# Performance work log

Hardware: AMD Instinct MI355X
Metric: run time of the kernel (lower is better)

The kernel has to match this reference:

```python
import jax, jax.numpy as jnp
import numpy as np

B, S, D, H, NUM_REL = 8, 1024, 1024, 16, 512
HD = D // H  # head size = 64


def setup_inputs() -> dict:
    key = jax.random.key(0)
    ks = jax.random.split(key, 12)
    sc = 0.02  # weight init scale for numerical stability
    inp = {
        "query": jax.random.normal(ks[0], (B, S, D), jnp.float32),
        "key": jax.random.normal(ks[1], (B, S, D), jnp.float32),
        "value": jax.random.normal(ks[2], (B, S, D), jnp.float32),
        "Wq": jax.random.normal(ks[3], (D, D), jnp.float32) * sc,
        "bq": jnp.zeros((D,), jnp.float32),
        "Wk": jax.random.normal(ks[4], (D, D), jnp.float32) * sc,
        "bk": jnp.zeros((D,), jnp.float32),
        "Wv": jax.random.normal(ks[5], (D, D), jnp.float32) * sc,
        "bv": jnp.zeros((D,), jnp.float32),
        "Wo": jax.random.normal(ks[6], (D, D), jnp.float32) * sc,
        "bo": jnp.zeros((D,), jnp.float32),
        "pos_table": jax.random.normal(ks[7], (NUM_REL, HD), jnp.float32) * sc,
        # True = masked position (causal: cannot attend to future)
        "mask": jnp.broadcast_to(jnp.triu(jnp.ones((S, S), bool), k=1), (B, S, S)),
    }
    return inp


def reference(query, key, value, Wq, bq, Wk, bk, Wv, bv, Wo, bo, pos_table, mask):
    Bq, Sq, Dm = query.shape
    hd = Dm // H

    def proj(x, W, b):
        # nn.Linear: x @ W.T + b, then split heads -> [B, H, S, hd]
        return (x @ W.T + b).reshape(Bq, Sq, H, hd).transpose(0, 2, 1, 3)

    q = proj(query, Wq, bq)
    k = proj(key, Wk, bk)
    v = proj(value, Wv, bv)

    scores = jnp.einsum("bhid,bhjd->bhij", q, k)

    # relative-position bias: idxs[i,j] = clip(i - j, 0, NUM_REL-1)
    t = jnp.arange(Sq)
    idxs = jnp.clip(t[:, None] - t[None, :], 0, pos_table.shape[0] - 1)
    pos = pos_table[idxs]  # [S, S, hd]
    scores = scores + jnp.einsum("bhid,ijd->bhij", q, pos)

    scores = scores / np.sqrt(hd).astype(np.float32)
    scores = jnp.where(mask[:, None, :, :], jnp.float32(-1e9), scores)
    prob = jax.nn.softmax(scores, axis=-1)  # dropout p=0.0 -> identity

    out = jnp.einsum("bhij,bhjd->bhid", prob, v)
    out = out.transpose(0, 2, 1, 3).reshape(Bq, Sq, Dm)
    return out @ Wo.T + bo
```

## Files before the change

### kernel.cpp

```cpp
#include <hip/hip_runtime.h>
#include <stdint.h>

#define DEV __device__ __forceinline__

typedef unsigned short u16;
typedef __bf16 bf16x8 __attribute__((ext_vector_type(8)));
typedef float  f32x4  __attribute__((ext_vector_type(4)));
typedef unsigned short u16x8 __attribute__((ext_vector_type(8)));
typedef unsigned short u16x4 __attribute__((ext_vector_type(4)));
typedef float  fvec4  __attribute__((ext_vector_type(4)));

constexpr int Sz   = 1024;
constexpr int Dm   = 1024;
constexpr int HDm  = 64;
constexpr int NREL = 512;
constexpr int Mrows = 8192;
constexpr int KV   = 32;

DEV u16 f2bf(float f) { return __builtin_bit_cast(u16, (__bf16)f); }
DEV float bf2f(u16 h) { return __builtin_bit_cast(float, (uint32_t)h << 16); }
DEV f32x4 mfma16(bf16x8 a, bf16x8 b, f32x4 c) {
  return __builtin_amdgcn_mfma_f32_16x16x32_bf16(a, b, c, 0, 0, 0);
}
DEV float ex2(float x) {
  float r;
  asm("v_exp_f32 %0, %1" : "=v"(r) : "v"(x));
  return r;
}

DEV u16x4 tr0(const u16* p) {
  u16x4 d;
  asm volatile("ds_read_b64_tr_b16 %0, %1"
               : "=v"(d)
               : "v"((const __attribute__((address_space(3))) u16*)p));
  return d;
}
DEV u16x4 tr512(const u16* p) {
  u16x4 d;
  asm volatile("ds_read_b64_tr_b16 %0, %1 offset:512"
               : "=v"(d)
               : "v"((const __attribute__((address_space(3))) u16*)p));
  return d;
}
DEV bf16x8 mk8(u16x4 a, u16x4 b) {
  u16x8 r;
  r[0] = a[0]; r[1] = a[1]; r[2] = a[2]; r[3] = a[3];
  r[4] = b[0]; r[5] = b[1]; r[6] = b[2]; r[7] = b[3];
  return __builtin_bit_cast(bf16x8, r);
}
DEV void gload(const u16* src, u16* dst) {
  __builtin_amdgcn_global_load_lds(
      (const __attribute__((address_space(1))) void*)src,
      (__attribute__((address_space(3))) void*)dst, 16, 0, 0);
}

__global__ __launch_bounds__(256) void cvt_kernel(const float* __restrict__ in,
                                                  u16* __restrict__ out) {
  size_t i = (size_t)blockIdx.x * 256 + threadIdx.x;
  fvec4 v = *(const fvec4*)(in + i * 4);
  u16x4 o;
  o[0] = f2bf(v[0]); o[1] = f2bf(v[1]); o[2] = f2bf(v[2]); o[3] = f2bf(v[3]);
  *(u16x4*)(out + i * 4) = o;
}

template<bool OUT_BF16>
__global__ __launch_bounds__(256) void gemm_bt(const u16* __restrict__ A,
                                               const u16* __restrict__ Bw,
                                               const float* __restrict__ bias,
                                               void* __restrict__ Cout) {
  __shared__ u16 As[128 * 64];
  __shared__ u16 Bs[128 * 64];
  const int tid = threadIdx.x;
  const int wave = tid >> 6, lane = tid & 63;
  const int lr = lane & 15, lg = lane >> 4;
  const int m0 = blockIdx.y * 128, n0 = blockIdx.x * 128;
  const int wr = (wave >> 1) * 64, wc = (wave & 1) * 64;
  f32x4 acc[4][4] = {};
  for (int k0 = 0; k0 < Dm; k0 += 64) {
    #pragma unroll
    for (int it = 0; it < 4; ++it) {
      int chunk = it * 256 + wave * 64 + lane;
      int row = chunk >> 3, c16 = chunk & 7;
      gload(Bw + (size_t)(n0 + row) * Dm + k0 + ((c16 ^ (row & 7)) * 8),
            &Bs[(it * 256 + wave * 64) * 8]);
      gload(A + (size_t)(m0 + row) * Dm + k0 + ((c16 ^ (row & 7)) * 8),
            &As[(it * 256 + wave * 64) * 8]);
    }
    __syncthreads();
    #pragma unroll
    for (int kk = 0; kk < 2; ++kk) {
      bf16x8 af[4], bf_[4];
      #pragma unroll
      for (int m = 0; m < 4; ++m)
        af[m] = *(const bf16x8*)&As[(wr + m * 16 + lr) * 64 + (((kk * 4 + lg) ^ (lr & 7)) * 8)];
      #pragma unroll
      for (int n = 0; n < 4; ++n)
        bf_[n] = *(const bf16x8*)&Bs[(wc + n * 16 + lr) * 64 + (((kk * 4 + lg) ^ (lr & 7)) * 8)];
      #pragma unroll
      for (int m = 0; m < 4; ++m)
        #pragma unroll
        for (int n = 0; n < 4; ++n)
          acc[m][n] = mfma16(af[m], bf_[n], acc[m][n]);
    }
    __syncthreads();
  }
  float bv[4];
  #pragma unroll
  for (int n = 0; n < 4; ++n) bv[n] = bias[n0 + wc + n * 16 + lr];
  #pragma unroll
  for (int m = 0; m < 4; ++m) {
    #pragma unroll
    for (int n = 0; n < 4; ++n) {
      const int gcol = n0 + wc + n * 16 + lr;
      #pragma unroll
      for (int r = 0; r < 4; ++r) {
        const int grow = m0 + wr + m * 16 + lg * 4 + r;
        float v = acc[m][n][r] + bv[n];
        if (OUT_BF16)
          ((u16*)Cout)[(size_t)grow * Dm + gcol] = f2bf(v);
        else
          ((float*)Cout)[(size_t)grow * Dm + gcol] = v;
      }
    }
  }
}

__global__ __launch_bounds__(256, 4) void attn_kernel(const u16* __restrict__ Q,
                                                      const u16* __restrict__ Kb,
                                                      const u16* __restrict__ Vb,
                                                      const u16* __restrict__ posB,
                                                      u16* __restrict__ O) {
  __shared__ u16 Ks[2][KV * 64];
  __shared__ u16 Vs[2][KV * 64];
  __shared__ u16 ring[128 * 64];
  __shared__ u16 SH[4][16 * 40];

  const int tid = threadIdx.x;
  const int wave = tid >> 6, lane = tid & 63;
  const int lr = lane & 15, lg = lane >> 4;
  const int bid = blockIdx.x;
  const int xcd = bid & 7;
  const int idx = bid >> 3;
  const int bhl = idx & 15;
  const int pp_ = idx >> 4;
  const int bh  = xcd * 16 + bhl;
  const int b = bh >> 4, h = bh & 15;

  u16* SHW = SH[wave];
  const size_t rowbase = (size_t)(b * Sz) * Dm + h * HDm;

  const int krow = tid >> 3, kc = tid & 7;
  const int vj = ((tid >> 5) << 2) | ((tid >> 1) & 3);
  const int vd = ((tid >> 3) & 3) * 16 + (tid & 1) * 8;
  const int rrow = tid >> 3, rcol = tid & 7;

  auto issueKV = [&](int t) {
    const int j0 = t * KV;
    const int bsel = t & 1;
    gload(Kb + rowbase + (size_t)(j0 + krow) * Dm + ((kc ^ (krow & 7)) * 8),
          &Ks[bsel][wave * 512]);
    gload(Vb + rowbase + (size_t)(j0 + vj) * Dm + vd, &Vs[bsel][wave * 512]);
  };
  auto stageRing = [&](int cb) {
    const int rel = cb + rrow;
    const int slot = rel & 127;
    const int cl = rel < 0 ? 0 : (rel > NREL - 1 ? NREL - 1 : rel);
    gload(posB + cl * 64 + ((rcol ^ (slot & 7)) * 8),
          &ring[((cb & 127) + wave * 8) * 64]);
  };

  constexpr float SC = 0.125f * 1.44269504f;

  for (int job = 0; job < 2; ++job) {
    const int qi = job ? pp_ : 15 - pp_;
    const int qb = qi * 64;
    const int wq = qb + wave * 16;
    const int nt = 2 * qi + 2;
    const int qg = wq + lr;

    const u16* qptr = Q + rowbase + (size_t)(wq + lr) * Dm;
    bf16x8 qf[2];
    qf[0] = *(const bf16x8*)(qptr + lg * 8);
    qf[1] = *(const bf16x8*)(qptr + 32 + lg * 8);

    float b511;
    {
      const u16* pp = posB + (NREL - 1) * HDm;
      bf16x8 pa0 = *(const bf16x8*)(pp + lg * 8);
      bf16x8 pa1 = *(const bf16x8*)(pp + 32 + lg * 8);
      f32x4 a = {};
      a = mfma16(pa0, qf[0], a);
      a = mfma16(pa1, qf[1], a);
      b511 = a[0];
    }

    stageRing(qb + 32);
    stageRing(qb);
    stageRing(qb - 32);
    issueKV(0);

    f32x4 oacc[4] = {};
    float m_i = -1e30f, l_i = 0.f;

    for (int t = 0; t < nt; ++t) {
      const int j0 = t * KV;
      const int bsel = t & 1;
      const bool active = (j0 <= wq + 15);
      const bool clamp = (wq - j0 - 31) >= NREL - 1;
      const int wb = wq - j0 - 31;

      if (t + 1 < nt) {
        stageRing(qb - 32 * (t + 1) - 32);
        issueKV(t + 1);
        asm volatile("s_waitcnt vmcnt(3)" ::: "memory");
      } else {
        asm volatile("s_waitcnt vmcnt(0)" ::: "memory");
      }
      __builtin_amdgcn_s_barrier();

      if (active) {
        if (!clamp) {
          #pragma unroll
          for (int wg = 0; wg < 3; ++wg) {
            const int rrel = wb + wg * 16 + lr;
            const int slot = rrel & 127;
            const u16* rp = &ring[slot * 64];
            f32x4 a = {};
            a = mfma16(qf[0], *(const bf16x8*)&rp[((0 + lg) ^ (slot & 7)) * 8], a);
            a = mfma16(qf[1], *(const bf16x8*)&rp[((4 + lg) ^ (slot & 7)) * 8], a);
            #pragma unroll
            for (int r = 0; r < 4; ++r) {
              const int q = lg * 4 + r;
              const int col = q - (wg * 16 + lr) + 31;
              if (col >= 0 && col < 32)
                SHW[q * 40 + col] = f2bf(a[r]);
            }
          }
        }

        __builtin_amdgcn_s_setprio(1);
        f32x4 s0 = {}, s1 = {};
        const u16* KT = &Ks[bsel][0];
        s0 = mfma16(*(const bf16x8*)&KT[(0 + lr) * 64 + (((0 + lg) ^ (lr & 7)) * 8)], qf[0], s0);
        s0 = mfma16(*(const bf16x8*)&KT[(0 + lr) * 64 + (((4 + lg) ^ (lr & 7)) * 8)], qf[1], s0);
        s1 = mfma16(*(const bf16x8*)&KT[(16 + lr) * 64 + (((0 + lg) ^ (lr & 7)) * 8)], qf[0], s1);
        s1 = mfma16(*(const bf16x8*)&KT[(16 + lr) * 64 + (((4 + lg) ^ (lr & 7)) * 8)], qf[1], s1);
        __builtin_amdgcn_s_setprio(0);

        float p0[4], p1[4];
        float tmax = -3e38f;
        if (clamp) {
          #pragma unroll
          for (int r = 0; r < 4; ++r) {
            p0[r] = (s0[r] + b511) * SC; tmax = fmaxf(tmax, p0[r]);
            p1[r] = (s1[r] + b511) * SC; tmax = fmaxf(tmax, p1[r]);
          }
        } else {
          u16x4 bv0 = *(const u16x4*)&SHW[lr * 40 + lg * 4];
          u16x4 bv1 = *(const u16x4*)&SHW[lr * 40 + 16 + lg * 4];
          #pragma unroll
          for (int r = 0; r < 4; ++r) {
            float v0 = (s0[r] + bf2f(bv0[r])) * SC;
            if (j0 + lg * 4 + r > qg) v0 = -1e9f;
            p0[r] = v0; tmax = fmaxf(tmax, v0);
            float v1 = (s1[r] + bf2f(bv1[r])) * SC;
            if (j0 + 16 + lg * 4 + r > qg) v1 = -1e9f;
            p1[r] = v1; tmax = fmaxf(tmax, v1);
          }
        }
        tmax = fmaxf(tmax, __shfl_xor(tmax, 16));
        tmax = fmaxf(tmax, __shfl_xor(tmax, 32));

        if (!__all(tmax <= m_i + 11.5f)) {
          float mn = fmaxf(m_i, tmax);
          float sc = ex2(m_i - mn);
          m_i = mn; l_i *= sc;
          #pragma unroll
          for (int dg = 0; dg < 4; ++dg) oacc[dg] *= sc;
        }

        float lsum = 0.f;
        #pragma unroll
        for (int r = 0; r < 4; ++r) {
          p0[r] = ex2(p0[r] - m_i); lsum += p0[r];
          p1[r] = ex2(p1[r] - m_i); lsum += p1[r];
        }
        lsum += __shfl_xor(lsum, 16);
        lsum += __shfl_xor(lsum, 32);
        l_i += lsum;

        u16x4 pk0, pk1;
        #pragma unroll
        for (int r = 0; r < 4; ++r) { pk0[r] = f2bf(p0[r]); pk1[r] = f2bf(p1[r]); }
        *(u16x4*)&SHW[lr * 40 + lg * 4] = pk0;
        *(u16x4*)&SHW[lr * 40 + 16 + lg * 4] = pk1;

        bf16x8 pB = *(const bf16x8*)&SHW[lr * 40 + lg * 8];

        u16x4 va[4][2];
        #pragma unroll
        for (int dg = 0; dg < 4; ++dg) {
          const u16* base = &Vs[bsel][(2 * lg) * 256 + dg * 64 + lr * 4];
          va[dg][0] = tr0(base);
          va[dg][1] = tr512(base);
        }
        asm volatile("s_waitcnt lgkmcnt(0)" ::: "memory");
        __builtin_amdgcn_sched_barrier(0);
        __builtin_amdgcn_s_setprio(1);
        #pragma unroll
        for (int dg = 0; dg < 4; ++dg)
          oacc[dg] = mfma16(mk8(va[dg][0], va[dg][1]), pB, oacc[dg]);
        __builtin_amdgcn_s_setprio(0);
      }
      __builtin_amdgcn_s_barrier();
    }

    const float inv = 1.0f / l_i;
    const size_t obase = rowbase + (size_t)qg * Dm;
    #pragma unroll
    for (int dg = 0; dg < 4; ++dg) {
      u16x4 w;
      #pragma unroll
      for (int r = 0; r < 4; ++r) w[r] = f2bf(oacc[dg][r] * inv);
      *(u16x4*)&O[obase + dg * 16 + lg * 4] = w;
    }
  }
}

extern "C" void kernel_launch(void* const* d_in, const int* in_sizes, int n_in,
                              void* d_out, int out_size, void* d_ws, size_t ws_size,
                              hipStream_t stream) {
  const float* query = (const float*)d_in[0];
  const float* key   = (const float*)d_in[1];
  const float* value = (const float*)d_in[2];
  const float* Wq    = (const float*)d_in[3];
  const float* bq    = (const float*)d_in[4];
  const float* Wk    = (const float*)d_in[5];
  const float* bk    = (const float*)d_in[6];
  const float* Wv    = (const float*)d_in[7];
  const float* bv    = (const float*)d_in[8];
  const float* Wo    = (const float*)d_in[9];
  const float* bo    = (const float*)d_in[10];
  const float* pos   = (const float*)d_in[11];

  char* ws = (char*)d_ws;
  u16* WqB  = (u16*)(ws);
  u16* WkB  = (u16*)(ws + (2ull << 20));
  u16* WvB  = (u16*)(ws + (4ull << 20));
  u16* WoB  = (u16*)(ws + (6ull << 20));
  u16* posB = (u16*)(ws + (8ull << 20));
  u16* Xq   = (u16*)(ws + (9ull << 20));
  u16* Xk   = (u16*)(ws + (25ull << 20));
  u16* Xv   = (u16*)(ws + (41ull << 20));
  u16* Qb   = (u16*)(ws + (57ull << 20));
  u16* Kb   = (u16*)(ws + (73ull << 20));
  u16* Vb   = Xk;
  u16* Ob   = Xq;

  cvt_kernel<<<1024, 256, 0, stream>>>(Wq, WqB);
  cvt_kernel<<<1024, 256, 0, stream>>>(Wk, WkB);
  cvt_kernel<<<1024, 256, 0, stream>>>(Wv, WvB);
  cvt_kernel<<<1024, 256, 0, stream>>>(Wo, WoB);
  cvt_kernel<<<32,   256, 0, stream>>>(pos, posB);
  cvt_kernel<<<8192, 256, 0, stream>>>(query, Xq);
  cvt_kernel<<<8192, 256, 0, stream>>>(key,   Xk);
  cvt_kernel<<<8192, 256, 0, stream>>>(value, Xv);

  dim3 ggrid(Dm / 128, Mrows / 128);
  gemm_bt<true><<<ggrid, 256, 0, stream>>>(Xq, WqB, bq, Qb);
  gemm_bt<true><<<ggrid, 256, 0, stream>>>(Xk, WkB, bk, Kb);
  gemm_bt<true><<<ggrid, 256, 0, stream>>>(Xv, WvB, bv, Vb);

  attn_kernel<<<1024, 256, 0, stream>>>(Qb, Kb, Vb, posB, Ob);

  gemm_bt<false><<<ggrid, 256, 0, stream>>>(Ob, WoB, bo, d_out);
}
```

Baseline: 215.2 us.

## Double-buffer GEMM tiles, batch QKV projections and conversions into single launches

Restructures the projection GEMM to double-buffer LDS tiles with async global-to-LDS loads, partial vmcnt waits and MFMA priority hints, so loads overlap compute. Adds XCD-aware block remapping for L2 locality. Merges the three input conversion kernels and, when the workspace is large enough, the three QKV GEMMs into single launches to cut launch overhead and tail effects. Doubles LDS per GEMM block, which may reduce occupancy.

New measurement: 192.2 us. 10.7% less time.

```diff
diff --git a/kernel.cpp b/kernel.cpp
--- a/kernel.cpp
+++ b/kernel.cpp
@@ -63,47 +63,79 @@
   *(u16x4*)(out + i * 4) = o;
 }
 
+__global__ __launch_bounds__(256) void cvt3_kernel(const float* __restrict__ a,
+                                                   const float* __restrict__ b,
+                                                   const float* __restrict__ c,
+                                                   u16* __restrict__ oa,
+                                                   u16* __restrict__ ob,
+                                                   u16* __restrict__ oc) {
+  const int bid = blockIdx.x;
+  const int seg = bid >> 13;
+  const float* in = seg == 0 ? a : seg == 1 ? b : c;
+  u16* out = seg == 0 ? oa : seg == 1 ? ob : oc;
+  size_t i = (size_t)(bid & 8191) * 256 + threadIdx.x;
+  fvec4 v = *(const fvec4*)(in + i * 4);
+  u16x4 o;
+  o[0] = f2bf(v[0]); o[1] = f2bf(v[1]); o[2] = f2bf(v[2]); o[3] = f2bf(v[3]);
+  *(u16x4*)(out + i * 4) = o;
+}
+
 template<bool OUT_BF16>
-__global__ __launch_bounds__(256) void gemm_bt(const u16* __restrict__ A,
-                                               const u16* __restrict__ Bw,
-                                               const float* __restrict__ bias,
-                                               void* __restrict__ Cout) {
-  __shared__ u16 As[128 * 64];
-  __shared__ u16 Bs[128 * 64];
+DEV void gemm_body(const u16* __restrict__ A, const u16* __restrict__ Bw,
+                   const float* __restrict__ bias, void* __restrict__ Cout,
+                   int m0, int n0, u16* As, u16* Bs) {
   const int tid = threadIdx.x;
   const int wave = tid >> 6, lane = tid & 63;
   const int lr = lane & 15, lg = lane >> 4;
-  const int m0 = blockIdx.y * 128, n0 = blockIdx.x * 128;
   const int wr = (wave >> 1) * 64, wc = (wave & 1) * 64;
-  f32x4 acc[4][4] = {};
-  for (int k0 = 0; k0 < Dm; k0 += 64) {
+
+  auto issue = [&](int t) {
+    const int k0 = t * 64;
+    u16* Ad = As + (t & 1) * (128 * 64);
+    u16* Bd = Bs + (t & 1) * (128 * 64);
     #pragma unroll
     for (int it = 0; it < 4; ++it) {
-      int chunk = it * 256 + wave * 64 + lane;
+      int chunk = it * 256 + tid;
       int row = chunk >> 3, c16 = chunk & 7;
       gload(Bw + (size_t)(n0 + row) * Dm + k0 + ((c16 ^ (row & 7)) * 8),
-            &Bs[(it * 256 + wave * 64) * 8]);
+            Bd + (it * 256 + wave * 64) * 8);
       gload(A + (size_t)(m0 + row) * Dm + k0 + ((c16 ^ (row & 7)) * 8),
-            &As[(it * 256 + wave * 64) * 8]);
-    }
-    __syncthreads();
+            Ad + (it * 256 + wave * 64) * 8);
+    }
+  };
+
+  issue(0);
+  f32x4 acc[4][4] = {};
+  for (int t = 0; t < 16; ++t) {
+    if (t < 15) {
+      issue(t + 1);
+      asm volatile("s_waitcnt vmcnt(8)" ::: "memory");
+    } else {
+      asm volatile("s_waitcnt vmcnt(0)" ::: "memory");
+    }
+    __builtin_amdgcn_s_barrier();
+    const u16* Ab = As + (t & 1) * (128 * 64);
+    const u16* Bb = Bs + (t & 1) * (128 * 64);
     #pragma unroll
     for (int kk = 0; kk < 2; ++kk) {
       bf16x8 af[4], bf_[4];
       #pragma unroll
       for (int m = 0; m < 4; ++m)
-        af[m] = *(const bf16x8*)&As[(wr + m * 16 + lr) * 64 + (((kk * 4 + lg) ^ (lr & 7)) * 8)];
+        af[m] = *(const bf16x8*)&Ab[(wr + m * 16 + lr) * 64 + (((kk * 4 + lg) ^ (lr & 7)) * 8)];
       #pragma unroll
       for (int n = 0; n < 4; ++n)
-        bf_[n] = *(const bf16x8*)&Bs[(wc + n * 16 + lr) * 64 + (((kk * 4 + lg) ^ (lr & 7)) * 8)];
+        bf_[n] = *(const bf16x8*)&Bb[(wc + n * 16 + lr) * 64 + (((kk * 4 + lg) ^ (lr & 7)) * 8)];
+      __builtin_amdgcn_s_setprio(1);
       #pragma unroll
       for (int m = 0; m < 4; ++m)
         #pragma unroll
         for (int n = 0; n < 4; ++n)
           acc[m][n] = mfma16(af[m], bf_[n], acc[m][n]);
-    }
-    __syncthreads();
+      __builtin_amdgcn_s_setprio(0);
+    }
+    __builtin_amdgcn_s_barrier();
   }
+
   float bv[4];
   #pragma unroll
   for (int n = 0; n < 4; ++n) bv[n] = bias[n0 + wc + n * 16 + lr];
@@ -123,6 +155,40 @@
       }
     }
   }
+}
+
+template<bool OUT_BF16>
+__global__ __launch_bounds__(256) void gemm1_kernel(const u16* __restrict__ A,
+                                                    const u16* __restrict__ Bw,
+                                                    const float* __restrict__ bias,
+                                                    void* __restrict__ Cout) {
+  __shared__ u16 As[2 * 128 * 64];
+  __shared__ u16 Bs[2 * 128 * 64];
+  const int r = blockIdx.x;
+  const int xcd = r & 7, loc = r >> 3;
+  const int m0 = (xcd * 8 + (loc & 7)) * 128;
+  const int n0 = (loc >> 3) * 128;
+  gemm_body<OUT_BF16>(A, Bw, bias, Cout, m0, n0, As, Bs);
+}
+
+__global__ __launch_bounds__(256) void gemm3_kernel(
+    const u16* __restrict__ Xq, const u16* __restrict__ Xk, const u16* __restrict__ Xv,
+    const u16* __restrict__ Wq, const u16* __restrict__ Wk, const u16* __restrict__ Wv,
+    const float* __restrict__ bq, const float* __restrict__ bk, const float* __restrict__ bv,
+    u16* __restrict__ Cq, u16* __restrict__ Ck, u16* __restrict__ Cv) {
+  __shared__ u16 As[2 * 128 * 64];
+  __shared__ u16 Bs[2 * 128 * 64];
+  const int flat = blockIdx.x;
+  const int seg = flat >> 9;
+  const int r = flat & 511;
+  const int xcd = r & 7, loc = r >> 3;
+  const int m0 = (xcd * 8 + (loc & 7)) * 128;
+  const int n0 = (loc >> 3) * 128;
+  const u16* A = seg == 0 ? Xq : seg == 1 ? Xk : Xv;
+  const u16* Bw = seg == 0 ? Wq : seg == 1 ? Wk : Wv;
+  const float* bias = seg == 0 ? bq : seg == 1 ? bk : bv;
+  u16* C = seg == 0 ? Cq : seg == 1 ? Ck : Cv;
+  gemm_body<true>(A, Bw, bias, C, m0, n0, As, Bs);
 }
 
 __global__ __launch_bounds__(256, 4) void attn_kernel(const u16* __restrict__ Q,
@@ -354,24 +420,28 @@
   u16* Xv   = (u16*)(ws + (41ull << 20));
   u16* Qb   = (u16*)(ws + (57ull << 20));
   u16* Kb   = (u16*)(ws + (73ull << 20));
-  u16* Vb   = Xk;
   u16* Ob   = Xq;
+
+  const bool bigws = ws_size >= (105ull << 20);
+  u16* Vb = bigws ? (u16*)(ws + (89ull << 20)) : Xk;
 
   cvt_kernel<<<1024, 256, 0, stream>>>(Wq, WqB);
   cvt_kernel<<<1024, 256, 0, stream>>>(Wk, WkB);
   cvt_kernel<<<1024, 256, 0, stream>>>(Wv, WvB);
   cvt_kernel<<<1024, 256, 0, stream>>>(Wo, WoB);
   cvt_kernel<<<32,   256, 0, stream>>>(pos, posB);
-  cvt_kernel<<<8192, 256, 0, stream>>>(query, Xq);
-  cvt_kernel<<<8192, 256, 0, stream>>>(key,   Xk);
-  cvt_kernel<<<8192, 256, 0, stream>>>(value, Xv);
-
-  dim3 ggrid(Dm / 128, Mrows / 128);
-  gemm_bt<true><<<ggrid, 256, 0, stream>>>(Xq, WqB, bq, Qb);
-  gemm_bt<true><<<ggrid, 256, 0, stream>>>(Xk, WkB, bk, Kb);
-  gemm_bt<true><<<ggrid, 256, 0, stream>>>(Xv, WvB, bv, Vb);
+  cvt3_kernel<<<24576, 256, 0, stream>>>(query, key, value, Xq, Xk, Xv);
+
+  if (bigws) {
+    gemm3_kernel<<<1536, 256, 0, stream>>>(Xq, Xk, Xv, WqB, WkB, WvB,
+                                           bq, bk, bv, Qb, Kb, Vb);
+  } else {
+    gemm1_kernel<true><<<512, 256, 0, stream>>>(Xq, WqB, bq, Qb);
+    gemm1_kernel<true><<<512, 256, 0, stream>>>(Xk, WkB, bk, Kb);
+    gemm1_kernel<true><<<512, 256, 0, stream>>>(Xv, WvB, bv, Vb);
+  }
 
   attn_kernel<<<1024, 256, 0, stream>>>(Qb, Kb, Vb, posB, Ob);
 
-  gemm_bt<false><<<ggrid, 256, 0, stream>>>(Ob, WoB, bo, d_out);
-}
+  gemm1_kernel<false><<<512, 256, 0, stream>>>(Ob, WoB, bo, d_out);
+}
```
